# Optimization experiments

Hardware: AMD Instinct MI355X
Metric: run time of the kernel (lower is better)

The kernel has to match this reference:

```python
import jax, jax.numpy as jnp
import numpy as np
import math

D_MODEL = 1024
N_HEADS = 16
D_K = D_MODEL // N_HEADS
D_FF = 4096
B, T = 1, 4096
EPS = 1e-5


def _layer_norm(x, g, b):
    mu = jnp.mean(x, axis=-1, keepdims=True)
    var = jnp.mean(jnp.square(x - mu), axis=-1, keepdims=True)
    return (x - mu) * jax.lax.rsqrt(var + EPS) * g + b


def setup_inputs() -> dict:
    key = jax.random.key(0)
    ks = jax.random.split(key, 8)
    s = 0.02
    return {
        "x": jax.random.normal(ks[0], (B, T, D_MODEL), dtype=jnp.float32),
        "ln1_g": jnp.ones((D_MODEL,), jnp.float32),
        "ln1_b": jnp.zeros((D_MODEL,), jnp.float32),
        "w_qkv": jax.random.normal(ks[1], (3 * D_MODEL, D_MODEL), jnp.float32) * s,
        "b_qkv": jnp.zeros((3 * D_MODEL,), jnp.float32),
        "w_out": jax.random.normal(ks[2], (D_MODEL, D_MODEL), jnp.float32) * s,
        "b_out": jnp.zeros((D_MODEL,), jnp.float32),
        "ln2_g": jnp.ones((D_MODEL,), jnp.float32),
        "ln2_b": jnp.zeros((D_MODEL,), jnp.float32),
        "w1": jax.random.normal(ks[3], (D_FF, D_MODEL), jnp.float32) * s,
        "b1": jnp.zeros((D_FF,), jnp.float32),
        "w2": jax.random.normal(ks[4], (D_MODEL, D_FF), jnp.float32) * s,
        "b2": jnp.zeros((D_MODEL,), jnp.float32),
    }


def reference(x, ln1_g, ln1_b, w_qkv, b_qkv, w_out, b_out, ln2_g, ln2_b, w1, b1, w2, b2):
    Bx, Tx, C = x.shape
    # --- attention (pre-norm) ---
    h = _layer_norm(x, ln1_g, ln1_b)
    qkv = h @ w_qkv.T + b_qkv                      # [B,T,3C]
    q, k, v = jnp.split(qkv, 3, axis=-1)
    def heads(t):  # [B,T,C] -> [B,H,T,dk]
        return t.reshape(Bx, Tx, N_HEADS, D_K).transpose(0, 2, 1, 3)
    q, k, v = heads(q), heads(k), heads(v)
    scale = math.sqrt(D_K)
    scores = jnp.einsum("bhqd,bhkd->bhqk", q, k) / scale
    causal = jnp.triu(jnp.ones((Tx, Tx), dtype=bool), k=1)
    scores = jnp.where(causal[None, None], -jnp.inf, scores)
    attn_weights = jax.nn.softmax(scores, axis=-1)  # [B,H,T,T]
    out = jnp.einsum("bhqk,bhkd->bhqd", attn_weights, v)
    out = out.transpose(0, 2, 1, 3).reshape(Bx, Tx, C)
    attn_out = out @ w_out.T + b_out
    x = x + attn_out
    # --- FFN (pre-norm) ---
    h2 = _layer_norm(x, ln2_g, ln2_b)
    ff = jax.nn.gelu(h2 @ w1.T + b1, approximate=False) @ w2.T + b2
    x = x + ff
    return (x, attn_weights)
```

## Files before the change

kernel.cpp:

```cpp
#include <hip/hip_runtime.h>
#include <math.h>

typedef unsigned short u16;
typedef unsigned int u32;
typedef __attribute__((ext_vector_type(8))) short bf16x8;
typedef __attribute__((ext_vector_type(4))) float f32x4;

#define MFMA16(a, b, c) __builtin_amdgcn_mfma_f32_16x16x32_bf16((a), (b), (c), 0, 0, 0)

__device__ __forceinline__ u16 f2bf(float f) {
  u32 u = __float_as_uint(f);
  return (u16)((u + 0x7fffu + ((u >> 16) & 1u)) >> 16);
}

typedef const __attribute__((address_space(1))) u32* gas_t;
typedef __attribute__((address_space(3))) u32* las_t;
__device__ __forceinline__ void gl_lds16(const u16* g, u16* l) {
  __builtin_amdgcn_global_load_lds((gas_t)g, (las_t)l, 16, 0, 0);
}

__global__ __launch_bounds__(256) void cvt_all_kernel(const float* __restrict__ s0, u16* __restrict__ d0,
                                                      const float* __restrict__ s1, u16* __restrict__ d1,
                                                      const float* __restrict__ s2, u16* __restrict__ d2,
                                                      const float* __restrict__ s3, u16* __restrict__ d3) {
  int blk = blockIdx.x, t = threadIdx.x;
  const float* src;
  u16* dst;
  int i;
  if (blk < 3072)      { src = s0; dst = d0; i = blk * 256 + t; }
  else if (blk < 4096) { src = s1; dst = d1; i = (blk - 3072) * 256 + t; }
  else if (blk < 8192) { src = s2; dst = d2; i = (blk - 4096) * 256 + t; }
  else                 { src = s3; dst = d3; i = (blk - 8192) * 256 + t; }
  float4 v = ((const float4*)src)[i];
  ushort4 o;
  o.x = f2bf(v.x); o.y = f2bf(v.y); o.z = f2bf(v.z); o.w = f2bf(v.w);
  ((ushort4*)dst)[i] = o;
}

__global__ __launch_bounds__(256) void ln_kernel(const float* __restrict__ x,
                                                 const float* __restrict__ g,
                                                 const float* __restrict__ b,
                                                 u16* __restrict__ out) {
  int row = blockIdx.x, tid = threadIdx.x;
  float4 v = ((const float4*)(x + (size_t)row * 1024))[tid];
  float s = v.x + v.y + v.z + v.w;
  float s2 = v.x * v.x + v.y * v.y + v.z * v.z + v.w * v.w;
  for (int off = 32; off; off >>= 1) { s += __shfl_xor(s, off); s2 += __shfl_xor(s2, off); }
  __shared__ float ps[4], ps2[4];
  int wave = tid >> 6;
  if ((tid & 63) == 0) { ps[wave] = s; ps2[wave] = s2; }
  __syncthreads();
  float fs = ps[0] + ps[1] + ps[2] + ps[3];
  float fs2 = ps2[0] + ps2[1] + ps2[2] + ps2[3];
  float mu = fs * (1.0f / 1024.0f);
  float var = fs2 * (1.0f / 1024.0f) - mu * mu;
  float rs = rsqrtf(var + 1e-5f);
  float4 gv = ((const float4*)g)[tid];
  float4 bv = ((const float4*)b)[tid];
  ushort4 o;
  o.x = f2bf((v.x - mu) * rs * gv.x + bv.x);
  o.y = f2bf((v.y - mu) * rs * gv.y + bv.y);
  o.z = f2bf((v.z - mu) * rs * gv.z + bv.z);
  o.w = f2bf((v.w - mu) * rs * gv.w + bv.w);
  ((ushort4*)(out + (size_t)row * 1024))[tid] = o;
}

__global__ __launch_bounds__(256) void vtrans_kernel(const u16* __restrict__ qkv,
                                                     u16* __restrict__ vt) {
  const int tt = blockIdx.x, h = blockIdx.y;
  __shared__ u16 tile[64 * 68];
  const int tid = threadIdx.x;
#pragma unroll
  for (int i = 0; i < 2; i++) {
    int c = i * 256 + tid;
    int trow = c >> 3, dc = c & 7;
    const u16* src = qkv + (size_t)(tt * 64 + trow) * 3072 + 2048 + h * 64 + dc * 8;
    uint4 v = *(const uint4*)src;
    *(uint2*)&tile[trow * 68 + dc * 8] = make_uint2(v.x, v.y);
    *(uint2*)&tile[trow * 68 + dc * 8 + 4] = make_uint2(v.z, v.w);
  }
  __syncthreads();
#pragma unroll
  for (int i = 0; i < 2; i++) {
    int c = i * 256 + tid;
    int d = c >> 3, tc = c & 7;
    ushort4 o0, o1;
    o0.x = tile[(tc * 8 + 0) * 68 + d]; o0.y = tile[(tc * 8 + 1) * 68 + d];
    o0.z = tile[(tc * 8 + 2) * 68 + d]; o0.w = tile[(tc * 8 + 3) * 68 + d];
    o1.x = tile[(tc * 8 + 4) * 68 + d]; o1.y = tile[(tc * 8 + 5) * 68 + d];
    o1.z = tile[(tc * 8 + 6) * 68 + d]; o1.w = tile[(tc * 8 + 7) * 68 + d];
    u16* dst = vt + (size_t)(h * 64 + d) * 4096 + tt * 64 + tc * 8;
    *(ushort4*)dst = o0;
    *(ushort4*)(dst + 4) = o1;
  }
}

template <int EPI>
__device__ __forceinline__ void gemm_body(const u16* __restrict__ A, const u16* __restrict__ B,
                                          const float* __restrict__ bias,
                                          const float* __restrict__ resid,
                                          void* __restrict__ Cout, int M, int N, int K,
                                          int bxi, int byi, u16* As, u16* Bs) {
  const int tid = threadIdx.x, lane = tid & 63, wave = tid >> 6;
  const int wr = wave >> 1, wc = wave & 1;
  const int bm = byi * 128, bn = bxi * 128;
  const int r = lane & 15, qd = lane >> 4;
  (void)M;

  const u16 *ag[2], *bg[2];
  u16 *al[2], *bl[2];
#pragma unroll
  for (int i = 0; i < 2; i++) {
    int C0 = wave * 128 + i * 64;
    int sc = C0 + lane;
    int row = sc >> 2;
    int q = (sc & 3) ^ ((row >> 1) & 3);
    ag[i] = A + (size_t)(bm + row) * K + q * 8;
    al[i] = &As[C0 * 8];
    bg[i] = B + (size_t)(bn + row) * K + q * 8;
    bl[i] = &Bs[C0 * 8];
  }
  const int swz = (r >> 1) & 3;
  f32x4 acc[4][4] = {};
  for (int k0 = 0; k0 < K; k0 += 32) {
#pragma unroll
    for (int i = 0; i < 2; i++) { gl_lds16(ag[i] + k0, al[i]); gl_lds16(bg[i] + k0, bl[i]); }
    __syncthreads();
    bf16x8 af[4], bfr[4];
#pragma unroll
    for (int mi = 0; mi < 4; mi++) {
      int row = wr * 64 + mi * 16 + r;
      af[mi] = *(const bf16x8*)&As[(row * 4 + (qd ^ swz)) * 8];
    }
#pragma unroll
    for (int ni = 0; ni < 4; ni++) {
      int row = wc * 64 + ni * 16 + r;
      bfr[ni] = *(const bf16x8*)&Bs[(row * 4 + (qd ^ swz)) * 8];
    }
#pragma unroll
    for (int mi = 0; mi < 4; mi++)
#pragma unroll
      for (int ni = 0; ni < 4; ni++)
        acc[mi][ni] = MFMA16(af[mi], bfr[ni], acc[mi][ni]);
    __syncthreads();
  }
  const int crow0 = bm + wr * 64 + qd * 4;
  const int ccol0 = bn + wc * 64 + r;
#pragma unroll
  for (int ni = 0; ni < 4; ni++) {
    int col = ccol0 + ni * 16;
    float bv = bias[col];
#pragma unroll
    for (int mi = 0; mi < 4; mi++) {
#pragma unroll
      for (int rg = 0; rg < 4; rg++) {
        int row = crow0 + mi * 16 + rg;
        float v = acc[mi][ni][rg] + bv;
        if (EPI == 1) v += resid[(size_t)row * N + col];
        if (EPI == 2) v = 0.5f * v * (1.0f + erff(v * 0.70710678118654752f));
        if (EPI == 1) ((float*)Cout)[(size_t)row * N + col] = v;
        else ((u16*)Cout)[(size_t)row * N + col] = f2bf(v);
      }
    }
  }
}

template <int EPI>
__global__ __launch_bounds__(256, 2) void gemm_bf16(const u16* __restrict__ A,
                                                    const u16* __restrict__ B,
                                                    const float* __restrict__ bias,
                                                    const float* __restrict__ resid,
                                                    void* __restrict__ Cout,
                                                    int M, int N, int K) {
  __shared__ u16 As[128 * 32];
  __shared__ u16 Bs[128 * 32];
  gemm_body<EPI>(A, B, bias, resid, Cout, M, N, K, blockIdx.x, blockIdx.y, As, Bs);
}

__global__ __launch_bounds__(256, 2) void attn_pass1(const u16* __restrict__ qkv,
                                                     const u16* __restrict__ vt,
                                                     u16* __restrict__ aout,
                                                     float* __restrict__ mstat,
                                                     float* __restrict__ lstat) {
  const int b = blockIdx.x;
  int h, qb;
  if (b < 256) { h = b >> 4; qb = b & 15; }
  else         { int b2 = b - 256; h = b2 >> 4; qb = 31 - (b2 & 15); }
  const int tid = threadIdx.x, lane = tid & 63, wave = tid >> 6;
  const int r = lane & 15, qd = lane >> 4;
  __shared__ u16 Qs[128 * 64];
  __shared__ u16 Ks[128 * 64];
  __shared__ u16 Vts[64 * 128];
  __shared__ u16 Ps[128 * 128];

#pragma unroll
  for (int i = 0; i < 4; i++) {
    int C0 = wave * 256 + i * 64;
    int sc = C0 + lane;
    int row = sc >> 3;
    int q = (sc & 7) ^ (row & 7);
    gl_lds16(qkv + (size_t)(qb * 128 + row) * 3072 + h * 64 + q * 8, &Qs[C0 * 8]);
  }
  const u16* kgb[4];
  u16* klds[4];
#pragma unroll
  for (int i = 0; i < 4; i++) {
    int g = i * 256 + tid;
    int row = g >> 3, qq = g & 7;
    kgb[i] = qkv + (size_t)row * 3072 + 1024 + h * 64 + qq * 8;
    klds[i] = &Ks[(row * 8 + (qq ^ (row & 7))) * 8];
  }
  const u16* vg[4];
  u16* vl[4];
#pragma unroll
  for (int i = 0; i < 4; i++) {
    int C0 = wave * 256 + i * 64;
    int sc = C0 + lane;
    int d = sc >> 4;
    int qq = (sc & 15) ^ (d & 15);
    vg[i] = vt + (size_t)(h * 64 + d) * 4096 + qq * 8;
    vl[i] = &Vts[C0 * 8];
  }
  uint4 kcur[4], knxt[4] = {};
#pragma unroll
  for (int i = 0; i < 4; i++) kcur[i] = *(const uint4*)kgb[i];
  asm volatile("s_waitcnt vmcnt(0) lgkmcnt(0)" ::: "memory");
  __builtin_amdgcn_s_barrier();

  bf16x8 qf[2][2];
#pragma unroll
  for (int ni = 0; ni < 2; ni++)
#pragma unroll
    for (int kk = 0; kk < 2; kk++) {
      int qrow = wave * 32 + ni * 16 + r;
      int qq = kk * 4 + qd;
      qf[ni][kk] = *(const bf16x8*)&Qs[(qrow * 8 + (qq ^ (qrow & 7))) * 8];
    }
  f32x4 ot[4][2] = {};
  float m_run[2] = {-INFINITY, -INFINITY};
  float l_run[2] = {0.f, 0.f};

  for (int kb = 0; kb <= qb; kb++) {
#pragma unroll
    for (int i = 0; i < 4; i++) *(uint4*)klds[i] = kcur[i];
#pragma unroll
    for (int i = 0; i < 4; i++) gl_lds16(vg[i] + kb * 128, vl[i]);
    __builtin_amdgcn_sched_barrier(0);
    if (kb < qb) {
#pragma unroll
      for (int i = 0; i < 4; i++) knxt[i] = *(const uint4*)(kgb[i] + (size_t)(kb + 1) * 393216);
    }
    asm volatile("s_waitcnt lgkmcnt(0)" ::: "memory");
    __builtin_amdgcn_s_barrier();
    f32x4 st[8][2] = {};
#pragma unroll
    for (int kk = 0; kk < 2; kk++) {
      bf16x8 kf[8];
#pragma unroll
      for (int mi = 0; mi < 8; mi++) {
        int krow = mi * 16 + r;
        int qq = kk * 4 + qd;
        kf[mi] = *(const bf16x8*)&Ks[(krow * 8 + (qq ^ (krow & 7))) * 8];
      }
#pragma unroll
      for (int mi = 0; mi < 8; mi++)
#pragma unroll
        for (int ni = 0; ni < 2; ni++)
          st[mi][ni] = MFMA16(kf[mi], qf[ni][kk], st[mi][ni]);
    }
    if (kb == qb) {
#pragma unroll
      for (int mi = 0; mi < 8; mi++) {
        int k0 = mi * 16 + qd * 4;
#pragma unroll
        for (int ni = 0; ni < 2; ni++) {
          int qloc = wave * 32 + ni * 16 + r;
#pragma unroll
          for (int rg = 0; rg < 4; rg++)
            if (k0 + rg > qloc) st[mi][ni][rg] = -INFINITY;
        }
      }
    }
    float mb[2], alpha[2];
#pragma unroll
    for (int ni = 0; ni < 2; ni++) {
      float mx = -INFINITY;
#pragma unroll
      for (int mi = 0; mi < 8; mi++)
        mx = fmaxf(mx, fmaxf(fmaxf(st[mi][ni][0], st[mi][ni][1]),
                             fmaxf(st[mi][ni][2], st[mi][ni][3])));
      mx = fmaxf(mx, __shfl_xor(mx, 16));
      mx = fmaxf(mx, __shfl_xor(mx, 32));
      float mn = fmaxf(m_run[ni], mx);
      alpha[ni] = __expf((m_run[ni] - mn) * 0.125f);
      m_run[ni] = mn;
      mb[ni] = mn;
    }
#pragma unroll
    for (int ni = 0; ni < 2; ni++) {
      int qrow = wave * 32 + ni * 16 + r;
      float ls = 0.f;
#pragma unroll
      for (int mi = 0; mi < 8; mi++) {
        float p0 = __expf((st[mi][ni][0] - mb[ni]) * 0.125f);
        float p1 = __expf((st[mi][ni][1] - mb[ni]) * 0.125f);
        float p2 = __expf((st[mi][ni][2] - mb[ni]) * 0.125f);
        float p3 = __expf((st[mi][ni][3] - mb[ni]) * 0.125f);
        ls += p0 + p1 + p2 + p3;
        ushort4 pk;
        pk.x = f2bf(p0); pk.y = f2bf(p1); pk.z = f2bf(p2); pk.w = f2bf(p3);
        int qq = mi * 2 + (qd >> 1);
        int sc = qrow * 16 + (qq ^ (qrow & 15));
        *(ushort4*)&Ps[sc * 8 + (qd & 1) * 4] = pk;
      }
      ls += __shfl_xor(ls, 16);
      ls += __shfl_xor(ls, 32);
      l_run[ni] = l_run[ni] * alpha[ni] + ls;
#pragma unroll
      for (int mi = 0; mi < 4; mi++) ot[mi][ni] = ot[mi][ni] * alpha[ni];
    }
    if (kb < qb) asm volatile("s_waitcnt vmcnt(4) lgkmcnt(0)" ::: "memory");
    else         asm volatile("s_waitcnt vmcnt(0) lgkmcnt(0)" ::: "memory");
    __builtin_amdgcn_s_barrier();
#pragma unroll
    for (int kk = 0; kk < 4; kk++) {
      bf16x8 vf[4], pf[2];
#pragma unroll
      for (int mi = 0; mi < 4; mi++) {
        int d = mi * 16 + r;
        int qq = kk * 4 + qd;
        vf[mi] = *(const bf16x8*)&Vts[(d * 16 + (qq ^ (d & 15))) * 8];
      }
#pragma unroll
      for (int ni = 0; ni < 2; ni++) {
        int qrow = wave * 32 + ni * 16 + r;
        int qq = kk * 4 + qd;
        pf[ni] = *(const bf16x8*)&Ps[(qrow * 16 + (qq ^ (qrow & 15))) * 8];
      }
#pragma unroll
      for (int mi = 0; mi < 4; mi++)
#pragma unroll
        for (int ni = 0; ni < 2; ni++)
          ot[mi][ni] = MFMA16(vf[mi], pf[ni], ot[mi][ni]);
    }
    asm volatile("s_waitcnt lgkmcnt(0)" ::: "memory");
    __builtin_amdgcn_s_barrier();
    if (kb < qb) {
#pragma unroll
      for (int i = 0; i < 4; i++) kcur[i] = knxt[i];
    }
  }
#pragma unroll
  for (int ni = 0; ni < 2; ni++) {
    float il = 1.0f / l_run[ni];
    int qg = qb * 128 + wave * 32 + ni * 16 + r;
    if (qd == 0) {
      mstat[h * 4096 + qg] = m_run[ni];
      lstat[h * 4096 + qg] = l_run[ni];
    }
#pragma unroll
    for (int mi = 0; mi < 4; mi++) {
      ushort4 o;
      o.x = f2bf(ot[mi][ni][0] * il);
      o.y = f2bf(ot[mi][ni][1] * il);
      o.z = f2bf(ot[mi][ni][2] * il);
      o.w = f2bf(ot[mi][ni][3] * il);
      *(ushort4*)&aout[(size_t)qg * 1024 + h * 64 + mi * 16 + qd * 4] = o;
    }
  }
}

__device__ __forceinline__ void pass2_body(const u16* __restrict__ qkv,
                                           const float* __restrict__ mstat,
                                           const float* __restrict__ lstat,
                                           float* __restrict__ attn, int qb, int h, int k0,
                                           u16* Qs, u16* Ks) {
  const int tid = threadIdx.x, lane = tid & 63, wave = tid >> 6;
  const int r = lane & 15, qd = lane >> 4;
  const bool has_compute = (k0 <= qb);
  bf16x8 qf[2][2];
  float mrow[2], ilrow[2];
  const u16* kg[4];
  u16* kl[4];
  if (has_compute) {
#pragma unroll
    for (int i = 0; i < 4; i++) {
      int C0 = wave * 256 + i * 64;
      int sc = C0 + lane;
      int row = sc >> 3;
      int q = (sc & 7) ^ (row & 7);
      gl_lds16(qkv + (size_t)(qb * 128 + row) * 3072 + h * 64 + q * 8, &Qs[C0 * 8]);
    }
#pragma unroll
    for (int i = 0; i < 4; i++) {
      int C0 = wave * 256 + i * 64;
      int sc = C0 + lane;
      int row = sc >> 3;
      int q = (sc & 7) ^ (row & 7);
      kg[i] = qkv + (size_t)row * 3072 + 1024 + h * 64 + q * 8;
      kl[i] = &Ks[C0 * 8];
    }
    __syncthreads();
#pragma unroll
    for (int ni = 0; ni < 2; ni++) {
#pragma unroll
      for (int kk = 0; kk < 2; kk++) {
        int qrow = wave * 32 + ni * 16 + r;
        int qq = kk * 4 + qd;
        qf[ni][kk] = *(const bf16x8*)&Qs[(qrow * 8 + (qq ^ (qrow & 7))) * 8];
      }
      int qg = qb * 128 + wave * 32 + ni * 16 + r;
      mrow[ni] = mstat[h * 4096 + qg];
      ilrow[ni] = 1.0f / lstat[h * 4096 + qg];
    }
  }
  float* ahead = attn + ((size_t)h << 24);
  for (int kb = k0; kb < k0 + 8; kb++) {
    if (kb <= qb) {
#pragma unroll
      for (int i = 0; i < 4; i++) gl_lds16(kg[i] + (size_t)kb * 128 * 3072, kl[i]);
      __syncthreads();
      f32x4 st[8][2] = {};
#pragma unroll
      for (int kk = 0; kk < 2; kk++) {
        bf16x8 kf[8];
#pragma unroll
        for (int mi = 0; mi < 8; mi++) {
          int krow = mi * 16 + r;
          int qq = kk * 4 + qd;
          kf[mi] = *(const bf16x8*)&Ks[(krow * 8 + (qq ^ (krow & 7))) * 8];
        }
#pragma unroll
        for (int mi = 0; mi < 8; mi++)
#pragma unroll
          for (int ni = 0; ni < 2; ni++)
            st[mi][ni] = MFMA16(kf[mi], qf[ni][kk], st[mi][ni]);
      }
#pragma unroll
      for (int ni = 0; ni < 2; ni++) {
        int qloc = wave * 32 + ni * 16 + r;
        size_t rowbase = (size_t)(qb * 128 + qloc) * 4096 + (size_t)kb * 128;
#pragma unroll
        for (int mi = 0; mi < 8; mi++) {
          int kk0 = mi * 16 + qd * 4;
          float v0, v1, v2, v3;
          v0 = __expf((st[mi][ni][0] - mrow[ni]) * 0.125f) * ilrow[ni];
          v1 = __expf((st[mi][ni][1] - mrow[ni]) * 0.125f) * ilrow[ni];
          v2 = __expf((st[mi][ni][2] - mrow[ni]) * 0.125f) * ilrow[ni];
          v3 = __expf((st[mi][ni][3] - mrow[ni]) * 0.125f) * ilrow[ni];
          if (kb == qb) {
            if (kk0 + 0 > qloc) v0 = 0.f;
            if (kk0 + 1 > qloc) v1 = 0.f;
            if (kk0 + 2 > qloc) v2 = 0.f;
            if (kk0 + 3 > qloc) v3 = 0.f;
          }
          *(float4*)(ahead + rowbase + kk0) = make_float4(v0, v1, v2, v3);
        }
      }
      __syncthreads();
    } else {
      size_t base = (size_t)(qb * 128) * 4096 + (size_t)kb * 128;
      float4 z = make_float4(0.f, 0.f, 0.f, 0.f);
#pragma unroll
      for (int i = 0; i < 16; i++) {
        int idx = i * 256 + tid;
        int ql = idx >> 5;
        int ko = (idx & 31) * 4;
        *(float4*)(ahead + base + (size_t)ql * 4096 + ko) = z;
      }
    }
  }
}

template <int EPI, int NXB, int GPG, int PPG, int PBASE>
__global__ __launch_bounds__(256, 2) void gemm_pass2_fused(
    const u16* __restrict__ A, const u16* __restrict__ B, const float* __restrict__ bias,
    const float* __restrict__ resid, void* __restrict__ Cout, int M, int N, int K,
    const u16* __restrict__ qkv, const float* __restrict__ mstat,
    const float* __restrict__ lstat, float* __restrict__ attn) {
  __shared__ u16 smem[128 * 64 * 2];
  constexpr int GRP = GPG + PPG;
  int idx = blockIdx.x;
  int grp = idx / GRP, rr = idx - grp * GRP;
  if (rr < GPG) {
    int g = grp * GPG + rr;
    gemm_body<EPI>(A, B, bias, resid, Cout, M, N, K, g % NXB, g / NXB, smem, smem + 128 * 32);
  } else {
    int p = PBASE + grp * PPG + (rr - GPG);
    pass2_body(qkv, mstat, lstat, attn, p & 31, (p >> 5) & 15, (p >> 9) * 8,
               smem, smem + 128 * 64);
  }
}

extern "C" void kernel_launch(void* const* d_in, const int* in_sizes, int n_in,
                              void* d_out, int out_size, void* d_ws, size_t ws_size,
                              hipStream_t stream) {
  const float* x     = (const float*)d_in[0];
  const float* ln1_g = (const float*)d_in[1];
  const float* ln1_b = (const float*)d_in[2];
  const float* w_qkv = (const float*)d_in[3];
  const float* b_qkv = (const float*)d_in[4];
  const float* w_out = (const float*)d_in[5];
  const float* b_out = (const float*)d_in[6];
  const float* ln2_g = (const float*)d_in[7];
  const float* ln2_b = (const float*)d_in[8];
  const float* w1    = (const float*)d_in[9];
  const float* b1    = (const float*)d_in[10];
  const float* w2    = (const float*)d_in[11];
  const float* b2    = (const float*)d_in[12];
  float* out_x = (float*)d_out;
  float* out_attn = out_x + (size_t)4096 * 1024;

  char* ws = (char*)d_ws;
  size_t off = 0;
  auto alloc = [&](size_t bytes) {
    void* p = ws + off;
    off += (bytes + 255) & ~(size_t)255;
    return p;
  };
  u16* WQKV = (u16*)alloc((size_t)3072 * 1024 * 2);
  u16* WOUT = (u16*)alloc((size_t)1024 * 1024 * 2);
  u16* W1   = (u16*)alloc((size_t)4096 * 1024 * 2);
  u16* W2   = (u16*)alloc((size_t)1024 * 4096 * 2);
  u16* H1   = (u16*)alloc((size_t)8388608);
  u16* QKV  = (u16*)alloc((size_t)25165824);
  u16* FF   = (u16*)alloc((size_t)33554432);
  u16* VT   = (u16*)alloc((size_t)8388608);
  float* MST = (float*)alloc((size_t)262144);
  float* LST = (float*)alloc((size_t)262144);
  u16* AOUT = (u16*)alloc((size_t)8388608);
  float* X1 = (float*)alloc((size_t)16777216);
  u16* H2  = (u16*)alloc((size_t)8388608);
  (void)ws_size; (void)in_sizes; (void)n_in; (void)out_size;

  cvt_all_kernel<<<12288, 256, 0, stream>>>(w_qkv, WQKV, w_out, WOUT, w1, W1, w2, W2);
  ln_kernel<<<4096, 256, 0, stream>>>(x, ln1_g, ln1_b, H1);
  gemm_bf16<0><<<dim3(24, 32), 256, 0, stream>>>(H1, WQKV, b_qkv, nullptr, QKV, 4096, 3072, 1024);
  vtrans_kernel<<<dim3(64, 16), 256, 0, stream>>>(QKV, VT);
  attn_pass1<<<512, 256, 0, stream>>>(QKV, VT, AOUT, MST, LST);
  gemm_bf16<1><<<dim3(8, 32), 256, 0, stream>>>(AOUT, WOUT, b_out, x, X1, 4096, 1024, 1024);
  ln_kernel<<<4096, 256, 0, stream>>>(X1, ln2_g, ln2_b, H2);
  gemm_pass2_fused<2, 32, 2, 1, 0><<<1536, 256, 0, stream>>>(
      H2, W1, b1, nullptr, FF, 4096, 4096, 1024, QKV, MST, LST, out_attn);
  gemm_pass2_fused<1, 8, 1, 6, 512><<<1792, 256, 0, stream>>>(
      FF, W2, b2, X1, out_x, 4096, 1024, 4096, QKV, MST, LST, out_attn);
}
```

Baseline: 1.589 ms.

## Move all attention-prob pass2 work into the FF2 fused kernel with full-row blocks

Pass2, which recomputes and writes the attention probabilities, is no longer split across the FF1 and FF2 kernels. FF1 becomes a plain GEMM, and all 512 pass2 blocks now run inside the FF2 kernel, interleaved two pass2 blocks per GEMM tile. Each pass2 block now handles a whole 32-key-block row instead of an 8-block chunk, so Q is loaded once per row and the chunk bookkeeping goes away. The cost is a less even load: row lengths differ under the causal mask, and FF1 no longer hides any of the attention writeback behind its compute.

```diff
diff --git a/kernel.cpp b/kernel.cpp
--- a/kernel.cpp
+++ b/kernel.cpp
@@ -373,49 +373,46 @@
 __device__ __forceinline__ void pass2_body(const u16* __restrict__ qkv,
                                            const float* __restrict__ mstat,
                                            const float* __restrict__ lstat,
-                                           float* __restrict__ attn, int qb, int h, int k0,
+                                           float* __restrict__ attn, int qb, int h,
                                            u16* Qs, u16* Ks) {
   const int tid = threadIdx.x, lane = tid & 63, wave = tid >> 6;
   const int r = lane & 15, qd = lane >> 4;
-  const bool has_compute = (k0 <= qb);
+#pragma unroll
+  for (int i = 0; i < 4; i++) {
+    int C0 = wave * 256 + i * 64;
+    int sc = C0 + lane;
+    int row = sc >> 3;
+    int q = (sc & 7) ^ (row & 7);
+    gl_lds16(qkv + (size_t)(qb * 128 + row) * 3072 + h * 64 + q * 8, &Qs[C0 * 8]);
+  }
+  const u16* kg[4];
+  u16* kl[4];
+#pragma unroll
+  for (int i = 0; i < 4; i++) {
+    int C0 = wave * 256 + i * 64;
+    int sc = C0 + lane;
+    int row = sc >> 3;
+    int q = (sc & 7) ^ (row & 7);
+    kg[i] = qkv + (size_t)row * 3072 + 1024 + h * 64 + q * 8;
+    kl[i] = &Ks[C0 * 8];
+  }
+  __syncthreads();
   bf16x8 qf[2][2];
   float mrow[2], ilrow[2];
-  const u16* kg[4];
-  u16* kl[4];
-  if (has_compute) {
-#pragma unroll
-    for (int i = 0; i < 4; i++) {
-      int C0 = wave * 256 + i * 64;
-      int sc = C0 + lane;
-      int row = sc >> 3;
-      int q = (sc & 7) ^ (row & 7);
-      gl_lds16(qkv + (size_t)(qb * 128 + row) * 3072 + h * 64 + q * 8, &Qs[C0 * 8]);
-    }
-#pragma unroll
-    for (int i = 0; i < 4; i++) {
-      int C0 = wave * 256 + i * 64;
-      int sc = C0 + lane;
-      int row = sc >> 3;
-      int q = (sc & 7) ^ (row & 7);
-      kg[i] = qkv + (size_t)row * 3072 + 1024 + h * 64 + q * 8;
-      kl[i] = &Ks[C0 * 8];
-    }
-    __syncthreads();
-#pragma unroll
-    for (int ni = 0; ni < 2; ni++) {
-#pragma unroll
-      for (int kk = 0; kk < 2; kk++) {
-        int qrow = wave * 32 + ni * 16 + r;
-        int qq = kk * 4 + qd;
-        qf[ni][kk] = *(const bf16x8*)&Qs[(qrow * 8 + (qq ^ (qrow & 7))) * 8];
-      }
-      int qg = qb * 128 + wave * 32 + ni * 16 + r;
-      mrow[ni] = mstat[h * 4096 + qg];
-      ilrow[ni] = 1.0f / lstat[h * 4096 + qg];
-    }
+#pragma unroll
+  for (int ni = 0; ni < 2; ni++) {
+#pragma unroll
+    for (int kk = 0; kk < 2; kk++) {
+      int qrow = wave * 32 + ni * 16 + r;
+      int qq = kk * 4 + qd;
+      qf[ni][kk] = *(const bf16x8*)&Qs[(qrow * 8 + (qq ^ (qrow & 7))) * 8];
+    }
+    int qg = qb * 128 + wave * 32 + ni * 16 + r;
+    mrow[ni] = mstat[h * 4096 + qg];
+    ilrow[ni] = 1.0f / lstat[h * 4096 + qg];
   }
   float* ahead = attn + ((size_t)h << 24);
-  for (int kb = k0; kb < k0 + 8; kb++) {
+  for (int kb = 0; kb < 32; kb++) {
     if (kb <= qb) {
 #pragma unroll
       for (int i = 0; i < 4; i++) gl_lds16(kg[i] + (size_t)kb * 128 * 3072, kl[i]);
@@ -442,19 +439,19 @@
         size_t rowbase = (size_t)(qb * 128 + qloc) * 4096 + (size_t)kb * 128;
 #pragma unroll
         for (int mi = 0; mi < 8; mi++) {
-          int kk0 = mi * 16 + qd * 4;
+          int k0 = mi * 16 + qd * 4;
           float v0, v1, v2, v3;
           v0 = __expf((st[mi][ni][0] - mrow[ni]) * 0.125f) * ilrow[ni];
           v1 = __expf((st[mi][ni][1] - mrow[ni]) * 0.125f) * ilrow[ni];
           v2 = __expf((st[mi][ni][2] - mrow[ni]) * 0.125f) * ilrow[ni];
           v3 = __expf((st[mi][ni][3] - mrow[ni]) * 0.125f) * ilrow[ni];
           if (kb == qb) {
-            if (kk0 + 0 > qloc) v0 = 0.f;
-            if (kk0 + 1 > qloc) v1 = 0.f;
-            if (kk0 + 2 > qloc) v2 = 0.f;
-            if (kk0 + 3 > qloc) v3 = 0.f;
+            if (k0 + 0 > qloc) v0 = 0.f;
+            if (k0 + 1 > qloc) v1 = 0.f;
+            if (k0 + 2 > qloc) v2 = 0.f;
+            if (k0 + 3 > qloc) v3 = 0.f;
           }
-          *(float4*)(ahead + rowbase + kk0) = make_float4(v0, v1, v2, v3);
+          *(float4*)(ahead + rowbase + k0) = make_float4(v0, v1, v2, v3);
         }
       }
       __syncthreads();
@@ -472,23 +469,20 @@
   }
 }
 
-template <int EPI, int NXB, int GPG, int PPG, int PBASE>
-__global__ __launch_bounds__(256, 2) void gemm_pass2_fused(
+__global__ __launch_bounds__(256, 2) void ff2_pass2_fused(
     const u16* __restrict__ A, const u16* __restrict__ B, const float* __restrict__ bias,
-    const float* __restrict__ resid, void* __restrict__ Cout, int M, int N, int K,
+    const float* __restrict__ resid, float* __restrict__ Cout,
     const u16* __restrict__ qkv, const float* __restrict__ mstat,
     const float* __restrict__ lstat, float* __restrict__ attn) {
   __shared__ u16 smem[128 * 64 * 2];
-  constexpr int GRP = GPG + PPG;
   int idx = blockIdx.x;
-  int grp = idx / GRP, rr = idx - grp * GRP;
-  if (rr < GPG) {
-    int g = grp * GPG + rr;
-    gemm_body<EPI>(A, B, bias, resid, Cout, M, N, K, g % NXB, g / NXB, smem, smem + 128 * 32);
+  int q3 = idx / 3, r3 = idx - q3 * 3;
+  if (r3 == 0) {
+    gemm_body<1>(A, B, bias, resid, (void*)Cout, 4096, 1024, 4096, q3 & 7, q3 >> 3,
+                 smem, smem + 128 * 32);
   } else {
-    int p = PBASE + grp * PPG + (rr - GPG);
-    pass2_body(qkv, mstat, lstat, attn, p & 31, (p >> 5) & 15, (p >> 9) * 8,
-               smem, smem + 128 * 64);
+    int p = q3 * 2 + (r3 - 1);
+    pass2_body(qkv, mstat, lstat, attn, p & 31, p >> 5, smem, smem + 128 * 64);
   }
 }
 
@@ -540,8 +534,6 @@
   attn_pass1<<<512, 256, 0, stream>>>(QKV, VT, AOUT, MST, LST);
   gemm_bf16<1><<<dim3(8, 32), 256, 0, stream>>>(AOUT, WOUT, b_out, x, X1, 4096, 1024, 1024);
   ln_kernel<<<4096, 256, 0, stream>>>(X1, ln2_g, ln2_b, H2);
-  gemm_pass2_fused<2, 32, 2, 1, 0><<<1536, 256, 0, stream>>>(
-      H2, W1, b1, nullptr, FF, 4096, 4096, 1024, QKV, MST, LST, out_attn);
-  gemm_pass2_fused<1, 8, 1, 6, 512><<<1792, 256, 0, stream>>>(
-      FF, W2, b2, X1, out_x, 4096, 1024, 4096, QKV, MST, LST, out_attn);
-}
+  gemm_bf16<2><<<dim3(32, 32), 256, 0, stream>>>(H2, W1, b1, nullptr, FF, 4096, 4096, 1024);
+  ff2_pass2_fused<<<768, 256, 0, stream>>>(FF, W2, b2, X1, out_x, QKV, MST, LST, out_attn);
+}
```

Measured after the change: 1.608 ms. No clear change (+1.2%).
